# Performance work log

Measured on AMD Instinct MI355X. Metric: run time of the kernel, lower is better.

The kernel has to match this reference:

```python
import jax, jax.numpy as jnp
import numpy as np

BIG_NEGATIVE_SCALAR = -10000.0
SEGMENT_SIZE = 64
DILATION = 2
D_K = 128
POS_EMB_SCALING = 1.0


def setup_inputs() -> dict:
    key = jax.random.key(0)
    k1, k2, k3, k4, k5 = jax.random.split(key, 5)
    B, T, E = 4, 8192, 1024
    d_k, d_v = 128, 128
    inv = 1.0 / np.sqrt(d_k)
    return {
        "x_in": jax.random.normal(k1, (B, T, E), dtype=jnp.float32),
        "P": jax.random.normal(k2, (T, T), dtype=jnp.float32),
        "Wk": jax.random.normal(k3, (d_k, E), dtype=jnp.float32) * inv,
        "Wq": jax.random.normal(k4, (d_k, E), dtype=jnp.float32) * inv,
        "Wv": jax.random.normal(k5, (d_v, E), dtype=jnp.float32) * inv,
    }


def reference(x_in, P, Wk, Wq, Wv):
    B, T, E = x_in.shape
    seg, dil = SEGMENT_SIZE, DILATION
    nseg = T // seg
    norm_fact = 1.0 / np.sqrt(D_K)
    d_v = Wv.shape[0]

    # [B, nseg, seg, E] -> [B, seg, E, nseg], then dilate along the segment axis
    x_view = x_in.reshape(B, nseg, seg, E).transpose(0, 2, 3, 1)
    x_dil = x_view[:, :, :, ::dil]                      # [B, seg, E, nseg_d]

    Q = jnp.einsum('ijkl,mk->ijlm', x_dil, Wq)          # [B, seg, nseg_d, d_k]
    K = jnp.einsum('ijkl,mk->ijlm', x_dil, Wk)
    V = jnp.einsum('ijkl,mk->ijlm', x_dil, Wv)          # [B, seg, nseg_d, d_v]

    KQ = jnp.einsum('ijkp,ijop->ijko', K, Q)            # [B, seg, nseg_d(key), nseg_d(query)]

    causal_mask = jnp.tril(jnp.ones((nseg, nseg), dtype=bool))[::dil, ::dil]
    KQ = jnp.where(causal_mask, KQ, BIG_NEGATIVE_SCALAR)

    # positional bias: P is [T, T]; segment-level bias at within-segment offset 0
    Ps = P * POS_EMB_SCALING
    p_bias = Ps.reshape(nseg, seg, nseg, seg)[::dil, :, ::dil, :][:, 0, :, 0]
    KQ = KQ + p_bias

    smKQ = jax.nn.softmax(KQ * norm_fact, axis=2)       # softmax over key axis
    att = jnp.einsum('ijld,ijlm->ijdm', smKQ, V)        # [B, seg, nseg_d, d_v]

    # 'same' padding: scatter dilated outputs back into full-length sequence
    res = jnp.zeros((B, T, d_v), dtype=x_in.dtype)
    res = res.at[:, ::dil, :].set(att.reshape(B, -1, d_v))
    return res
```

## Files before the change

kernel.cpp:

```cpp
#include <hip/hip_runtime.h>
#include <hip/hip_bf16.h>

#define B_  4
#define T_  8192
#define E_  1024
#define DK_ 128

typedef __attribute__((ext_vector_type(8))) _Float16 half8;
typedef __attribute__((ext_vector_type(4))) float float4v;

__device__ __forceinline__ half8 cvt8h(float4 a, float4 b) {
    half8 r;
    r[0] = (_Float16)a.x; r[1] = (_Float16)a.y; r[2] = (_Float16)a.z; r[3] = (_Float16)a.w;
    r[4] = (_Float16)b.x; r[5] = (_Float16)b.y; r[6] = (_Float16)b.z; r[7] = (_Float16)b.w;
    return r;
}

__global__ __launch_bounds__(512, 2)
void dilattn(const float* __restrict__ x_in, const float* __restrict__ P,
             const float* __restrict__ Wk, const float* __restrict__ Wq,
             const float* __restrict__ Wv, float* __restrict__ out)
{
    __shared__ float lds_f[16384];
    ushort* xs  = (ushort*)lds_f;
    ushort* wsm = xs + 64 * 72;
    constexpr int A_OFF   = 0;
    constexpr int B_OFF   = 8192;
    constexpr int S_OFF   = 8192;
    constexpr int DEN_OFF = 8192 + 4160;
    const float NORMF = 0.08838834764831845f;

    const int tid  = threadIdx.x;
    const int lane = tid & 63;
    const int w    = __builtin_amdgcn_readfirstlane(tid >> 6);
    const int b    = blockIdx.x >> 6;
    const int s    = blockIdx.x & 63;

    const int lr   = lane & 15;
    const int lg   = lane >> 4;
    const int mt   = w & 3;
    const int half = w >> 2;

    const int c8 = tid & 7;
    const int xr = tid >> 3;
    const float* xrow = x_in + ((size_t)b * T_ + 128 * xr + s) * E_ + c8 * 8;
    const float* wrow[6];
#pragma unroll
    for (int p = 0; p < 6; ++p) {
        const int r = xr + 64 * p;
        const float* base = (r < 128) ? (Wq + (size_t)r * E_)
                          : (r < 256) ? (Wk + (size_t)(r - 128) * E_)
                                      : (Wv + (size_t)(r - 256) * E_);
        wrow[p] = base + c8 * 8;
    }

    float4v acc[12];
#pragma unroll
    for (int j = 0; j < 12; ++j) acc[j] = (float4v){0.f, 0.f, 0.f, 0.f};

    float4 xa0, xa1, wa0[6], wa1[6];
    xa0 = *(const float4*)(xrow);
    xa1 = *(const float4*)(xrow + 4);
#pragma unroll
    for (int p = 0; p < 6; ++p) {
        wa0[p] = *(const float4*)(wrow[p]);
        wa1[p] = *(const float4*)(wrow[p] + 4);
    }

    for (int ki = 0; ki < 16; ++ki) {
        __syncthreads();
        *(half8*)&xs[xr * 72 + c8 * 8] = cvt8h(xa0, xa1);
#pragma unroll
        for (int p = 0; p < 6; ++p)
            *(half8*)&wsm[(xr + 64 * p) * 72 + c8 * 8] = cvt8h(wa0[p], wa1[p]);
        __syncthreads();

        if (ki < 15) {
            const int k0 = (ki + 1) * 64;
            xa0 = *(const float4*)(xrow + k0);
            xa1 = *(const float4*)(xrow + k0 + 4);
#pragma unroll
            for (int p = 0; p < 6; ++p) {
                wa0[p] = *(const float4*)(wrow[p] + k0);
                wa1[p] = *(const float4*)(wrow[p] + k0 + 4);
            }
        }

#pragma unroll
        for (int kk = 0; kk < 2; ++kk) {
            const half8 afr = *(const half8*)&xs[(mt * 16 + lr) * 72 + kk * 32 + lg * 8];
#pragma unroll
            for (int j = 0; j < 12; ++j) {
                const half8 bfr = *(const half8*)&wsm[((half * 12 + j) * 16 + lr) * 72 + kk * 32 + lg * 8];
                acc[j] = __builtin_amdgcn_mfma_f32_16x16x32_f16(afr, bfr, acc[j], 0, 0, 0);
            }
        }
    }
    __syncthreads();

    const int rbase = mt * 16 + lg * 4;
#pragma unroll
    for (int j = 0; j < 12; ++j) {
        const int nt = half * 12 + j;
        const int n  = nt * 16 + lr;
        if (nt < 8) {
#pragma unroll
            for (int r = 0; r < 4; ++r) {
                const int l = rbase + r;
                lds_f[A_OFF + l * 128 + ((n + 4 * l) & 127)] = acc[j][r];
            }
        } else if (nt < 16) {
            const int m = n - 128;
#pragma unroll
            for (int r = 0; r < 4; ++r) {
                const int l = rbase + r;
                lds_f[B_OFF + m * 64 + ((l + m) & 63)] = acc[j][r];
            }
        }
    }
    __syncthreads();

    float sd[8];
#pragma unroll
    for (int i = 0; i < 8; ++i) sd[i] = 0.f;

    for (int m4 = 0; m4 < 32; ++m4) {
        const int mm = 4 * m4;
        const float k0 = lds_f[B_OFF + (mm + 0) * 64 + ((lane + mm + 0) & 63)];
        const float k1 = lds_f[B_OFF + (mm + 1) * 64 + ((lane + mm + 1) & 63)];
        const float k2 = lds_f[B_OFF + (mm + 2) * 64 + ((lane + mm + 2) & 63)];
        const float k3 = lds_f[B_OFF + (mm + 3) * 64 + ((lane + mm + 3) & 63)];
#pragma unroll
        for (int i = 0; i < 8; ++i) {
            const int q = w * 8 + i;
            const float4 qv = *(const float4*)&lds_f[A_OFF + q * 128 + ((4 * (m4 + q)) & 127)];
            sd[i] = fmaf(k0, qv.x, fmaf(k1, qv.y, fmaf(k2, qv.z, fmaf(k3, qv.w, sd[i]))));
        }
    }
    __syncthreads();

#pragma unroll
    for (int i = 0; i < 8; ++i) {
        const int q = w * 8 + i;
        const float pb = P[(size_t)lane * ((size_t)128 * T_) + (size_t)q * 128];
        const float logit = ((lane >= q ? sd[i] : -10000.f) + pb) * NORMF;
        lds_f[S_OFF + lane * 65 + q] = logit;
    }
    if (half == 1) {
#pragma unroll
        for (int j = 4; j < 12; ++j) {
            const int nt = 12 + j;
            const int m  = nt * 16 + lr - 256;
#pragma unroll
            for (int r = 0; r < 4; ++r) {
                const int l = rbase + r;
                lds_f[A_OFF + l * 128 + ((m + 4 * l) & 127)] = acc[j][r];
            }
        }
    }
    __syncthreads();

    if (tid < 64) {
        const int q = tid;
        float mx = -3.402823466e38f;
        for (int k = 0; k < 64; ++k) mx = fmaxf(mx, lds_f[S_OFF + k * 65 + q]);
        float sum = 0.f;
        for (int k = 0; k < 64; ++k) {
            const float ev = __expf(lds_f[S_OFF + k * 65 + q] - mx);
            lds_f[S_OFF + k * 65 + q] = ev;
            sum += ev;
        }
        lds_f[DEN_OFF + q] = 1.0f / sum;
    }
    __syncthreads();

    float4 o0 = {0,0,0,0}, o1 = {0,0,0,0}, o2 = {0,0,0,0}, o3 = {0,0,0,0};
    for (int k = 0; k < 64; ++k) {
        const float p = lds_f[S_OFF + k * 65 + lane];
        const int base = A_OFF + k * 128;
        const float4 v0 = *(const float4*)&lds_f[base + ((16 * w + 0  + 4 * k) & 127)];
        const float4 v1 = *(const float4*)&lds_f[base + ((16 * w + 4  + 4 * k) & 127)];
        const float4 v2 = *(const float4*)&lds_f[base + ((16 * w + 8  + 4 * k) & 127)];
        const float4 v3 = *(const float4*)&lds_f[base + ((16 * w + 12 + 4 * k) & 127)];
        o0.x = fmaf(p, v0.x, o0.x); o0.y = fmaf(p, v0.y, o0.y); o0.z = fmaf(p, v0.z, o0.z); o0.w = fmaf(p, v0.w, o0.w);
        o1.x = fmaf(p, v1.x, o1.x); o1.y = fmaf(p, v1.y, o1.y); o1.z = fmaf(p, v1.z, o1.z); o1.w = fmaf(p, v1.w, o1.w);
        o2.x = fmaf(p, v2.x, o2.x); o2.y = fmaf(p, v2.y, o2.y); o2.z = fmaf(p, v2.z, o2.z); o2.w = fmaf(p, v2.w, o2.w);
        o3.x = fmaf(p, v3.x, o3.x); o3.y = fmaf(p, v3.y, o3.y); o3.z = fmaf(p, v3.z, o3.z); o3.w = fmaf(p, v3.w, o3.w);
    }
    const float inv = lds_f[DEN_OFF + lane];
    float* orow = out + ((size_t)b * T_ + (size_t)(2 * (s * 64 + lane))) * DK_ + w * 16;
    float4 r0 = {o0.x*inv, o0.y*inv, o0.z*inv, o0.w*inv};
    float4 r1 = {o1.x*inv, o1.y*inv, o1.z*inv, o1.w*inv};
    float4 r2 = {o2.x*inv, o2.y*inv, o2.z*inv, o2.w*inv};
    float4 r3 = {o3.x*inv, o3.y*inv, o3.z*inv, o3.w*inv};
    *(float4*)(orow + 0)  = r0;
    *(float4*)(orow + 4)  = r1;
    *(float4*)(orow + 8)  = r2;
    *(float4*)(orow + 12) = r3;
}

extern "C" void kernel_launch(void* const* d_in, const int* in_sizes, int n_in,
                              void* d_out, int out_size, void* d_ws, size_t ws_size,
                              hipStream_t stream) {
    (void)in_sizes; (void)n_in; (void)d_ws; (void)ws_size;
    const float* x_in = (const float*)d_in[0];
    const float* P    = (const float*)d_in[1];
    const float* Wk   = (const float*)d_in[2];
    const float* Wq   = (const float*)d_in[3];
    const float* Wv   = (const float*)d_in[4];
    float* out = (float*)d_out;

    hipMemsetAsync(d_out, 0, (size_t)out_size * sizeof(float), stream);
    dilattn<<<dim3(256), dim3(512), 0, stream>>>(x_in, P, Wk, Wq, Wv, out);
}
```

Measured before the change: 440.0 us.

## Pre-convert weights to fp16, double-buffer GEMM staging, warp-shuffle softmax, drop memset

A small pre-kernel converts Wq/Wk/Wv to fp16 in a tiled workspace layout each call, halving weight read traffic in the main kernel and removing per-block conversion. The projection loop is now double-buffered in LDS with two-stage register prefetch, cutting one barrier per step. Softmax is computed per wave with shuffle reductions instead of a single-wave serial loop, with normalization folded into the probabilities. The host memset is removed and the kernel writes zeros to the odd rows itself, at the cost of an extra kernel launch and larger LDS use that may limit occupancy.

```diff
diff --git a/kernel.cpp b/kernel.cpp
--- a/kernel.cpp
+++ b/kernel.cpp
@@ -1,5 +1,4 @@
 #include <hip/hip_runtime.h>
-#include <hip/hip_bf16.h>
 
 #define B_  4
 #define T_  8192
@@ -16,18 +15,31 @@
     return r;
 }
 
+__global__ void wconv(const float* __restrict__ Wk, const float* __restrict__ Wq,
+                      const float* __restrict__ Wv, ushort* __restrict__ W16) {
+    const int g   = blockIdx.x * 256 + threadIdx.x;
+    const int c   = g & 7;
+    const int ki  = (g >> 3) & 15;
+    const int row = g >> 7;
+    const float* src = (row < 128) ? (Wq + (size_t)row * E_)
+                     : (row < 256) ? (Wk + (size_t)(row - 128) * E_)
+                                   : (Wv + (size_t)(row - 256) * E_);
+    src += ki * 64 + c * 8;
+    *(half8*)(W16 + (size_t)(ki * 384 + row) * 64 + c * 8) =
+        cvt8h(*(const float4*)src, *(const float4*)(src + 4));
+}
+
 __global__ __launch_bounds__(512, 2)
 void dilattn(const float* __restrict__ x_in, const float* __restrict__ P,
-             const float* __restrict__ Wk, const float* __restrict__ Wq,
-             const float* __restrict__ Wv, float* __restrict__ out)
+             const ushort* __restrict__ W16, float* __restrict__ out)
 {
-    __shared__ float lds_f[16384];
-    ushort* xs  = (ushort*)lds_f;
-    ushort* wsm = xs + 64 * 72;
-    constexpr int A_OFF   = 0;
-    constexpr int B_OFF   = 8192;
-    constexpr int S_OFF   = 8192;
-    constexpr int DEN_OFF = 8192 + 4160;
+    __shared__ __align__(16) ushort sh[2 * 64 * 72 + 2 * 384 * 72];
+    ushort* xs0   = sh;
+    ushort* ws0   = sh + 2 * 64 * 72;
+    float*  lds_f = (float*)sh;
+    constexpr int A_OFF = 0;
+    constexpr int B_OFF = 8192;
+    constexpr int S_OFF = 8192;
     const float NORMF = 0.08838834764831845f;
 
     const int tid  = threadIdx.x;
@@ -43,60 +55,50 @@
 
     const int c8 = tid & 7;
     const int xr = tid >> 3;
-    const float* xrow = x_in + ((size_t)b * T_ + 128 * xr + s) * E_ + c8 * 8;
-    const float* wrow[6];
-#pragma unroll
-    for (int p = 0; p < 6; ++p) {
-        const int r = xr + 64 * p;
-        const float* base = (r < 128) ? (Wq + (size_t)r * E_)
-                          : (r < 256) ? (Wk + (size_t)(r - 128) * E_)
-                                      : (Wv + (size_t)(r - 256) * E_);
-        wrow[p] = base + c8 * 8;
-    }
+    const float*  xrow  = x_in + ((size_t)b * T_ + 128 * xr + s) * E_ + c8 * 8;
+    const ushort* wbase = W16 + xr * 64 + c8 * 8;
 
     float4v acc[12];
 #pragma unroll
     for (int j = 0; j < 12; ++j) acc[j] = (float4v){0.f, 0.f, 0.f, 0.f};
 
-    float4 xa0, xa1, wa0[6], wa1[6];
-    xa0 = *(const float4*)(xrow);
-    xa1 = *(const float4*)(xrow + 4);
-#pragma unroll
-    for (int p = 0; p < 6; ++p) {
-        wa0[p] = *(const float4*)(wrow[p]);
-        wa1[p] = *(const float4*)(wrow[p] + 4);
-    }
-
-    for (int ki = 0; ki < 16; ++ki) {
+    uint4  wr[2][6];
+    float4 xa[2][2];
+
+#define ISSUE_STAGE(K, SL) { \
+    _Pragma("unroll") \
+    for (int p = 0; p < 6; ++p) wr[SL][p] = *(const uint4*)(wbase + (K) * 24576 + p * 4096); \
+    xa[SL][0] = *(const float4*)(xrow + (K) * 64); \
+    xa[SL][1] = *(const float4*)(xrow + (K) * 64 + 4); }
+
+#define WRITE_STAGE(K, SL) { \
+    const int wb_ = ((K) & 1) * (384 * 72); \
+    _Pragma("unroll") \
+    for (int p = 0; p < 6; ++p) *(uint4*)&ws0[wb_ + (xr + 64 * p) * 72 + c8 * 8] = wr[SL][p]; \
+    *(half8*)&xs0[((K) & 1) * (64 * 72) + xr * 72 + c8 * 8] = cvt8h(xa[SL][0], xa[SL][1]); }
+
+    ISSUE_STAGE(0, 0);
+    ISSUE_STAGE(1, 1);
+    WRITE_STAGE(0, 0);
+    __syncthreads();
+
+#pragma unroll
+    for (int k = 0; k < 16; ++k) {
+        if (k < 14) ISSUE_STAGE(k + 2, k & 1);
+        if (k < 15) WRITE_STAGE(k + 1, (k + 1) & 1);
+        const int xb = (k & 1) * (64 * 72);
+        const int wb = (k & 1) * (384 * 72);
+#pragma unroll
+        for (int kk = 0; kk < 2; ++kk) {
+            const half8 afr = *(const half8*)&xs0[xb + (mt * 16 + lr) * 72 + kk * 32 + lg * 8];
+#pragma unroll
+            for (int j = 0; j < 12; ++j) {
+                const half8 bfr = *(const half8*)&ws0[wb + ((half * 12 + j) * 16 + lr) * 72 + kk * 32 + lg * 8];
+                acc[j] = __builtin_amdgcn_mfma_f32_16x16x32_f16(afr, bfr, acc[j], 0, 0, 0);
+            }
+        }
         __syncthreads();
-        *(half8*)&xs[xr * 72 + c8 * 8] = cvt8h(xa0, xa1);
-#pragma unroll
-        for (int p = 0; p < 6; ++p)
-            *(half8*)&wsm[(xr + 64 * p) * 72 + c8 * 8] = cvt8h(wa0[p], wa1[p]);
-        __syncthreads();
-
-        if (ki < 15) {
-            const int k0 = (ki + 1) * 64;
-            xa0 = *(const float4*)(xrow + k0);
-            xa1 = *(const float4*)(xrow + k0 + 4);
-#pragma unroll
-            for (int p = 0; p < 6; ++p) {
-                wa0[p] = *(const float4*)(wrow[p] + k0);
-                wa1[p] = *(const float4*)(wrow[p] + k0 + 4);
-            }
-        }
-
-#pragma unroll
-        for (int kk = 0; kk < 2; ++kk) {
-            const half8 afr = *(const half8*)&xs[(mt * 16 + lr) * 72 + kk * 32 + lg * 8];
-#pragma unroll
-            for (int j = 0; j < 12; ++j) {
-                const half8 bfr = *(const half8*)&wsm[((half * 12 + j) * 16 + lr) * 72 + kk * 32 + lg * 8];
-                acc[j] = __builtin_amdgcn_mfma_f32_16x16x32_f16(afr, bfr, acc[j], 0, 0, 0);
-            }
-        }
-    }
-    __syncthreads();
+    }
 
     const int rbase = mt * 16 + lg * 4;
 #pragma unroll
@@ -119,6 +121,11 @@
         }
     }
     __syncthreads();
+
+    float pb[8];
+#pragma unroll
+    for (int i = 0; i < 8; ++i)
+        pb[i] = P[(size_t)lane * ((size_t)128 * T_) + (size_t)(w * 8 + i) * 128];
 
     float sd[8];
 #pragma unroll
@@ -139,13 +146,6 @@
     }
     __syncthreads();
 
-#pragma unroll
-    for (int i = 0; i < 8; ++i) {
-        const int q = w * 8 + i;
-        const float pb = P[(size_t)lane * ((size_t)128 * T_) + (size_t)q * 128];
-        const float logit = ((lane >= q ? sd[i] : -10000.f) + pb) * NORMF;
-        lds_f[S_OFF + lane * 65 + q] = logit;
-    }
     if (half == 1) {
 #pragma unroll
         for (int j = 4; j < 12; ++j) {
@@ -158,19 +158,19 @@
             }
         }
     }
-    __syncthreads();
-
-    if (tid < 64) {
-        const int q = tid;
-        float mx = -3.402823466e38f;
-        for (int k = 0; k < 64; ++k) mx = fmaxf(mx, lds_f[S_OFF + k * 65 + q]);
-        float sum = 0.f;
-        for (int k = 0; k < 64; ++k) {
-            const float ev = __expf(lds_f[S_OFF + k * 65 + q] - mx);
-            lds_f[S_OFF + k * 65 + q] = ev;
-            sum += ev;
-        }
-        lds_f[DEN_OFF + q] = 1.0f / sum;
+
+#pragma unroll
+    for (int i = 0; i < 8; ++i) {
+        const int q = w * 8 + i;
+        const float logit = ((lane >= q ? sd[i] : -10000.f) + pb[i]) * NORMF;
+        float mx = logit;
+#pragma unroll
+        for (int off = 32; off >= 1; off >>= 1) mx = fmaxf(mx, __shfl_xor(mx, off));
+        const float ev = __expf(logit - mx);
+        float sum = ev;
+#pragma unroll
+        for (int off = 32; off >= 1; off >>= 1) sum += __shfl_xor(sum, off);
+        lds_f[S_OFF + lane * 65 + q] = ev * (1.0f / sum);
     }
     __syncthreads();
 
@@ -187,29 +187,30 @@
         o2.x = fmaf(p, v2.x, o2.x); o2.y = fmaf(p, v2.y, o2.y); o2.z = fmaf(p, v2.z, o2.z); o2.w = fmaf(p, v2.w, o2.w);
         o3.x = fmaf(p, v3.x, o3.x); o3.y = fmaf(p, v3.y, o3.y); o3.z = fmaf(p, v3.z, o3.z); o3.w = fmaf(p, v3.w, o3.w);
     }
-    const float inv = lds_f[DEN_OFF + lane];
     float* orow = out + ((size_t)b * T_ + (size_t)(2 * (s * 64 + lane))) * DK_ + w * 16;
-    float4 r0 = {o0.x*inv, o0.y*inv, o0.z*inv, o0.w*inv};
-    float4 r1 = {o1.x*inv, o1.y*inv, o1.z*inv, o1.w*inv};
-    float4 r2 = {o2.x*inv, o2.y*inv, o2.z*inv, o2.w*inv};
-    float4 r3 = {o3.x*inv, o3.y*inv, o3.z*inv, o3.w*inv};
-    *(float4*)(orow + 0)  = r0;
-    *(float4*)(orow + 4)  = r1;
-    *(float4*)(orow + 8)  = r2;
-    *(float4*)(orow + 12) = r3;
+    *(float4*)(orow + 0)  = o0;
+    *(float4*)(orow + 4)  = o1;
+    *(float4*)(orow + 8)  = o2;
+    *(float4*)(orow + 12) = o3;
+    const float4 z = {0.f, 0.f, 0.f, 0.f};
+    *(float4*)(orow + DK_ + 0)  = z;
+    *(float4*)(orow + DK_ + 4)  = z;
+    *(float4*)(orow + DK_ + 8)  = z;
+    *(float4*)(orow + DK_ + 12) = z;
 }
 
 extern "C" void kernel_launch(void* const* d_in, const int* in_sizes, int n_in,
                               void* d_out, int out_size, void* d_ws, size_t ws_size,
                               hipStream_t stream) {
-    (void)in_sizes; (void)n_in; (void)d_ws; (void)ws_size;
+    (void)in_sizes; (void)n_in; (void)out_size; (void)ws_size;
     const float* x_in = (const float*)d_in[0];
     const float* P    = (const float*)d_in[1];
     const float* Wk   = (const float*)d_in[2];
     const float* Wq   = (const float*)d_in[3];
     const float* Wv   = (const float*)d_in[4];
     float* out = (float*)d_out;
-
-    hipMemsetAsync(d_out, 0, (size_t)out_size * sizeof(float), stream);
-    dilattn<<<dim3(256), dim3(512), 0, stream>>>(x_in, P, Wk, Wq, Wv, out);
-}
+    ushort* W16 = (ushort*)d_ws;
+
+    wconv<<<dim3(192), dim3(256), 0, stream>>>(Wk, Wq, Wv, W16);
+    dilattn<<<dim3(256), dim3(512), 0, stream>>>(x_in, P, W16, out);
+}
```

Result: slower. 468.4 us (+6.5%).
